# Optimization experiments

Hardware: AMD Instinct MI355X
Metric: run time of the kernel (lower is better)

## Reference

```python
import math
import jax, jax.numpy as jnp
import numpy as np

D_MODEL = 1024
NUM_HEADS = 16
HEAD_DIM = D_MODEL // NUM_HEADS
CAUSAL = True


def setup_inputs() -> dict:
    key = jax.random.key(0)
    ks = jax.random.split(key, 9)
    B, S = 2, 2048
    s = 1.0 / math.sqrt(D_MODEL)
    x = jax.random.normal(ks[0], (B, S, D_MODEL), dtype=jnp.float32)
    Wq = jax.random.normal(ks[1], (D_MODEL, D_MODEL), dtype=jnp.float32) * s
    bq = jax.random.normal(ks[2], (D_MODEL,), dtype=jnp.float32) * 0.01
    Wk = jax.random.normal(ks[3], (D_MODEL, D_MODEL), dtype=jnp.float32) * s
    bk = jax.random.normal(ks[4], (D_MODEL,), dtype=jnp.float32) * 0.01
    Wv = jax.random.normal(ks[5], (D_MODEL, D_MODEL), dtype=jnp.float32) * s
    bv = jax.random.normal(ks[6], (D_MODEL,), dtype=jnp.float32) * 0.01
    Wo = jax.random.normal(ks[7], (D_MODEL, D_MODEL), dtype=jnp.float32) * s
    bo = jax.random.normal(ks[8], (D_MODEL,), dtype=jnp.float32) * 0.01
    return {"x": x, "Wq": Wq, "bq": bq, "Wk": Wk, "bk": bk,
            "Wv": Wv, "bv": bv, "Wo": Wo, "bo": bo}


def reference(x, Wq, bq, Wk, bk, Wv, bv, Wo, bo):
    B, S, _ = x.shape
    # projections (torch Linear: x @ W.T + b; here W already stored as [in,out])
    q = x @ Wq + bq
    k = x @ Wk + bk
    v = x @ Wv + bv
    # split heads -> [B, H, S, hd]
    def split(t):
        return t.reshape(B, S, NUM_HEADS, HEAD_DIM).transpose(0, 2, 1, 3)
    q, k, v = split(q), split(k), split(v)
    scores = jnp.einsum('bhqd,bhkd->bhqk', q, k) / math.sqrt(HEAD_DIM)
    if CAUSAL:
        causal = jnp.tril(jnp.ones((S, S), dtype=bool))  # True = keep
        scores = jnp.where(causal, scores, -jnp.inf)
    attn = jax.nn.softmax(scores, axis=-1)
    out = jnp.einsum('bhqk,bhkd->bhqd', attn, v)
    out = out.transpose(0, 2, 1, 3).reshape(B, S, D_MODEL)
    return out @ Wo + bo
```

## Files before the change

### kernel.cpp

```cpp
#include <hip/hip_runtime.h>
#include <hip/hip_bf16.h>

typedef __bf16 bf16_t;
typedef __bf16 v8bf __attribute__((ext_vector_type(8)));
typedef float  v4f  __attribute__((ext_vector_type(4)));

#define MFMA16(a, b, c) __builtin_amdgcn_mfma_f32_16x16x32_bf16((a), (b), (c), 0, 0, 0)

#define GLDS16(g, l) __builtin_amdgcn_global_load_lds(                         \
    (const __attribute__((address_space(1))) void*)(g),                        \
    (__attribute__((address_space(3))) void*)(l), 16, 0, 0)

#define B_SZ   2
#define SEQ    2048
#define DM     1024
#define NH     16
#define HD     64
#define M_TOT  4096

#define QSCALE 0.18033688011112043f

__global__ __launch_bounds__(256)
void conv_x_kernel(const float* __restrict__ src, bf16_t* __restrict__ dst)
{
    int i = (blockIdx.x * 256 + threadIdx.x) * 8;
    float4 a = *reinterpret_cast<const float4*>(src + i);
    float4 b = *reinterpret_cast<const float4*>(src + i + 4);
    union { bf16_t h[8]; int4 v; } u;
    u.h[0] = (bf16_t)a.x; u.h[1] = (bf16_t)a.y; u.h[2] = (bf16_t)a.z; u.h[3] = (bf16_t)a.w;
    u.h[4] = (bf16_t)b.x; u.h[5] = (bf16_t)b.y; u.h[6] = (bf16_t)b.z; u.h[7] = (bf16_t)b.w;
    *reinterpret_cast<int4*>(dst + i) = u.v;
}

__global__ __launch_bounds__(256)
void conv_wt_kernel(const float* __restrict__ Wq, const float* __restrict__ Wk,
                    const float* __restrict__ Wv, const float* __restrict__ Wo,
                    bf16_t* __restrict__ WqkvT, bf16_t* __restrict__ WoT)
{
    __shared__ float t[32][33];
    const int z = blockIdx.z;
    const float* src = (z == 0) ? Wq : (z == 1) ? Wk : (z == 2) ? Wv : Wo;
    bf16_t* dst = (z < 3) ? (WqkvT + (size_t)z * 1048576) : WoT;
    const int tx = threadIdx.x & 31, ty = threadIdx.x >> 5;
    const int c0 = blockIdx.x * 32, r0 = blockIdx.y * 32;
#pragma unroll
    for (int i = 0; i < 4; ++i)
        t[ty + i * 8][tx] = src[(size_t)(r0 + ty + i * 8) * DM + c0 + tx];
    __syncthreads();
#pragma unroll
    for (int i = 0; i < 4; ++i)
        dst[(size_t)(c0 + ty + i * 8) * DM + r0 + tx] = (bf16_t)t[tx][ty + i * 8];
}

__global__ __launch_bounds__(256)
void gemm_qkv_kernel(const bf16_t* __restrict__ A, const bf16_t* __restrict__ BT,
                     const float* __restrict__ b0, const float* __restrict__ b1,
                     const float* __restrict__ b2,
                     bf16_t* __restrict__ oQ, bf16_t* __restrict__ oK,
                     bf16_t* __restrict__ oV)
{
    __shared__ __align__(16) bf16_t As[2 * 128 * 64];
    __shared__ __align__(16) bf16_t Bs[2 * 128 * 64];

    const int tid  = threadIdx.x;
    const int lane = tid & 63;
    const int wave = tid >> 6;
    const int wm   = (wave >> 1) * 64;
    const int wn   = (wave & 1) * 64;
    const int quad = lane >> 4;
    const int l15  = lane & 15;
    const int l7   = l15 & 7;

    const int mat = blockIdx.x >> 3;
    const int n0  = (blockIdx.x & 7) * 128;
    const int m0  = blockIdx.y * 128;
    const bf16_t* Bmat = BT + (size_t)mat * 1048576;

    const bf16_t *ap[4], *bp[4];
#pragma unroll
    for (int i = 0; i < 4; ++i) {
        int cidx = (wave * 4 + i) * 64 + lane;
        int r = cidx >> 3;
        int c = (cidx & 7) ^ (r & 7);
        ap[i] = A    + (size_t)(m0 + r) * DM + c * 8;
        bp[i] = Bmat + (size_t)(n0 + r) * DM + c * 8;
    }

    const v4f vzero = {0.f, 0.f, 0.f, 0.f};
    v4f acc[4][4];
#pragma unroll
    for (int mt = 0; mt < 4; ++mt)
#pragma unroll
        for (int nt = 0; nt < 4; ++nt) acc[mt][nt] = vzero;

#pragma unroll
    for (int i = 0; i < 4; ++i) {
        GLDS16(ap[i], As + (wave * 4 + i) * 512);
        GLDS16(bp[i], Bs + (wave * 4 + i) * 512);
        ap[i] += 64; bp[i] += 64;
    }

    for (int it = 0; it < 16; ++it) {
        const int cur = it & 1, nxt = cur ^ 1;
        __syncthreads();
        if (it < 15) {
#pragma unroll
            for (int i = 0; i < 4; ++i) {
                GLDS16(ap[i], As + nxt * 8192 + (wave * 4 + i) * 512);
                GLDS16(bp[i], Bs + nxt * 8192 + (wave * 4 + i) * 512);
                ap[i] += 64; bp[i] += 64;
            }
        }
#pragma unroll
        for (int ks = 0; ks < 2; ++ks) {
            v8bf af[4], bfq[4];
#pragma unroll
            for (int mt = 0; mt < 4; ++mt)
                af[mt] = *reinterpret_cast<const v8bf*>(
                    &As[cur * 8192 + (wm + mt * 16 + l15) * 64 + ((ks * 4 + quad) ^ l7) * 8]);
#pragma unroll
            for (int nt = 0; nt < 4; ++nt)
                bfq[nt] = *reinterpret_cast<const v8bf*>(
                    &Bs[cur * 8192 + (wn + nt * 16 + l15) * 64 + ((ks * 4 + quad) ^ l7) * 8]);
#pragma unroll
            for (int mt = 0; mt < 4; ++mt)
#pragma unroll
                for (int nt = 0; nt < 4; ++nt)
                    acc[mt][nt] = MFMA16(bfq[nt], af[mt], acc[mt][nt]);
        }
    }

    const float* bias = (mat == 0) ? b0 : (mat == 1) ? b1 : b2;
    if (mat != 2) {
        bf16_t* dst = (mat == 0) ? oQ : oK;
        const float scale = (mat == 0) ? QSCALE : 1.0f;
        const int h = (n0 + wn) >> 6;
#pragma unroll
        for (int nt = 0; nt < 4; ++nt) {
            const int dbase = nt * 16 + quad * 4;
            float4 bv = *reinterpret_cast<const float4*>(bias + n0 + wn + dbase);
#pragma unroll
            for (int mt = 0; mt < 4; ++mt) {
                int srow = m0 + wm + mt * 16 + l15;
                int b = srow >> 11, s = srow & 2047;
                union { bf16_t hh[4]; int2 v; } u;
                u.hh[0] = (bf16_t)((acc[mt][nt][0] + bv.x) * scale);
                u.hh[1] = (bf16_t)((acc[mt][nt][1] + bv.y) * scale);
                u.hh[2] = (bf16_t)((acc[mt][nt][2] + bv.z) * scale);
                u.hh[3] = (bf16_t)((acc[mt][nt][3] + bv.w) * scale);
                *reinterpret_cast<int2*>(
                    dst + ((size_t)(b * NH + h) * SEQ + s) * HD + dbase) = u.v;
            }
        }
    } else {
#pragma unroll
        for (int nt = 0; nt < 4; ++nt) {
#pragma unroll
            for (int r = 0; r < 4; ++r) {
                int coln = n0 + wn + nt * 16 + quad * 4 + r;
                float bv = bias[coln];
                int h = coln >> 6, d = coln & 63;
#pragma unroll
                for (int mt = 0; mt < 4; ++mt) {
                    int srow = m0 + wm + mt * 16 + l15;
                    int b = srow >> 11, s = srow & 2047;
                    oV[((size_t)(b * NH + h) * HD + d) * SEQ + s] =
                        (bf16_t)(acc[mt][nt][r] + bv);
                }
            }
        }
    }
}

__global__ __launch_bounds__(256)
void gemm_o_kernel(const bf16_t* __restrict__ A, const bf16_t* __restrict__ BT,
                   const float* __restrict__ bias, float* __restrict__ out)
{
    __shared__ __align__(16) bf16_t As[2 * 128 * 64];
    __shared__ __align__(16) bf16_t Bs[2 * 64 * 64];

    const int tid  = threadIdx.x;
    const int lane = tid & 63;
    const int wave = tid >> 6;
    const int wm   = (wave >> 1) * 64;
    const int wn   = (wave & 1) * 32;
    const int quad = lane >> 4;
    const int l15  = lane & 15;
    const int l7   = l15 & 7;

    const int n0 = blockIdx.x * 64;
    const int m0 = blockIdx.y * 128;

    const bf16_t *ap[4], *bp[2];
#pragma unroll
    for (int i = 0; i < 4; ++i) {
        int cidx = (wave * 4 + i) * 64 + lane;
        int r = cidx >> 3;
        int c = (cidx & 7) ^ (r & 7);
        ap[i] = A + (size_t)(m0 + r) * DM + c * 8;
    }
#pragma unroll
    for (int i = 0; i < 2; ++i) {
        int cidx = (wave * 2 + i) * 64 + lane;
        int r = cidx >> 3;
        int c = (cidx & 7) ^ (r & 7);
        bp[i] = BT + (size_t)(n0 + r) * DM + c * 8;
    }

    const v4f vzero = {0.f, 0.f, 0.f, 0.f};
    v4f acc[4][2];
#pragma unroll
    for (int mt = 0; mt < 4; ++mt)
#pragma unroll
        for (int nt = 0; nt < 2; ++nt) acc[mt][nt] = vzero;

#pragma unroll
    for (int i = 0; i < 4; ++i) { GLDS16(ap[i], As + (wave * 4 + i) * 512); ap[i] += 64; }
#pragma unroll
    for (int i = 0; i < 2; ++i) { GLDS16(bp[i], Bs + (wave * 2 + i) * 512); bp[i] += 64; }

    for (int it = 0; it < 16; ++it) {
        const int cur = it & 1, nxt = cur ^ 1;
        __syncthreads();
        if (it < 15) {
#pragma unroll
            for (int i = 0; i < 4; ++i) {
                GLDS16(ap[i], As + nxt * 8192 + (wave * 4 + i) * 512);
                ap[i] += 64;
            }
#pragma unroll
            for (int i = 0; i < 2; ++i) {
                GLDS16(bp[i], Bs + nxt * 4096 + (wave * 2 + i) * 512);
                bp[i] += 64;
            }
        }
#pragma unroll
        for (int ks = 0; ks < 2; ++ks) {
            v8bf af[4], bfq[2];
#pragma unroll
            for (int mt = 0; mt < 4; ++mt)
                af[mt] = *reinterpret_cast<const v8bf*>(
                    &As[cur * 8192 + (wm + mt * 16 + l15) * 64 + ((ks * 4 + quad) ^ l7) * 8]);
#pragma unroll
            for (int nt = 0; nt < 2; ++nt)
                bfq[nt] = *reinterpret_cast<const v8bf*>(
                    &Bs[cur * 4096 + (wn + nt * 16 + l15) * 64 + ((ks * 4 + quad) ^ l7) * 8]);
#pragma unroll
            for (int mt = 0; mt < 4; ++mt)
#pragma unroll
                for (int nt = 0; nt < 2; ++nt)
                    acc[mt][nt] = MFMA16(af[mt], bfq[nt], acc[mt][nt]);
        }
    }

#pragma unroll
    for (int mt = 0; mt < 4; ++mt) {
#pragma unroll
        for (int nt = 0; nt < 2; ++nt) {
            int col = n0 + wn + nt * 16 + l15;
            float bv = bias[col];
#pragma unroll
            for (int r = 0; r < 4; ++r) {
                int row = m0 + wm + mt * 16 + quad * 4 + r;
                out[(size_t)row * DM + col] = acc[mt][nt][r] + bv;
            }
        }
    }
}

__global__ __launch_bounds__(256)
void attn_kernel(const bf16_t* __restrict__ Q, const bf16_t* __restrict__ K,
                 const bf16_t* __restrict__ Vt, bf16_t* __restrict__ O)
{
    __shared__ __align__(16) bf16_t Ks[2][64 * 64];
    __shared__ __align__(16) bf16_t Vs[2][64 * 64];
    __shared__ __align__(16) bf16_t Ps[64 * 72];

    const int tid  = threadIdx.x;
    const int lane = tid & 63;
    const int w    = tid >> 6;
    const int quad = lane >> 4;
    const int l15  = lane & 15;
    const int l7   = lane & 7;

    const int p  = blockIdx.x;
    const int bh = blockIdx.y;
    const size_t base = (size_t)bh * SEQ * HD;
    const bf16_t* Qg = Q  + base;
    const bf16_t* Kg = K  + base;
    const bf16_t* Vg = Vt + base;

    const int rr0 = tid >> 3;
    const int cc0 = (tid & 7) ^ (rr0 & 7);
    const int bO = bh >> 4, hO = bh & 15;
    const v4f vzero = {0.f, 0.f, 0.f, 0.f};

    for (int phase = 0; phase < 2; ++phase) {
        const int t  = phase ? (31 - p) : p;
        const int q0 = t * 64;
        const int qg = q0 + w * 16 + l15;

        v8bf qf[2];
        {
            const bf16_t* qrow = Qg + (size_t)qg * HD;
            qf[0] = *reinterpret_cast<const v8bf*>(qrow + quad * 8);
            qf[1] = *reinterpret_cast<const v8bf*>(qrow + 32 + quad * 8);
        }

        const bf16_t* kp0 = Kg + (size_t)rr0 * HD + cc0 * 8;
        const bf16_t* kp1 = kp0 + 32 * HD;
        const bf16_t* vp0 = Vg + (size_t)rr0 * SEQ + cc0 * 8;
        const bf16_t* vp1 = vp0 + (size_t)32 * SEQ;

        v4f acc_o[4];
#pragma unroll
        for (int dt = 0; dt < 4; ++dt) acc_o[dt] = vzero;
        float lrow = 0.f;

        __syncthreads();
        GLDS16(kp0, &Ks[0][w * 512]);
        GLDS16(kp1, &Ks[0][2048 + w * 512]);
        GLDS16(vp0, &Vs[0][w * 512]);
        GLDS16(vp1, &Vs[0][2048 + w * 512]);
        kp0 += 64 * HD;  kp1 += 64 * HD;  vp0 += 64;  vp1 += 64;

        for (int kt = 0; kt <= t; ++kt) {
            const int cur = kt & 1, nxt = cur ^ 1;
            __syncthreads();
            if (kt < t) {
                GLDS16(kp0, &Ks[nxt][w * 512]);
                GLDS16(kp1, &Ks[nxt][2048 + w * 512]);
                GLDS16(vp0, &Vs[nxt][w * 512]);
                GLDS16(vp1, &Vs[nxt][2048 + w * 512]);
                kp0 += 64 * HD;  kp1 += 64 * HD;  vp0 += 64;  vp1 += 64;
            }

            v4f st[4];
#pragma unroll
            for (int ktile = 0; ktile < 4; ++ktile) st[ktile] = vzero;
#pragma unroll
            for (int ks = 0; ks < 2; ++ks) {
                v8bf kb[4];
#pragma unroll
                for (int ktile = 0; ktile < 4; ++ktile)
                    kb[ktile] = *reinterpret_cast<const v8bf*>(
                        &Ks[cur][(ktile * 16 + l15) * 64 + ((ks * 4 + quad) ^ l7) * 8]);
#pragma unroll
                for (int ktile = 0; ktile < 4; ++ktile)
                    st[ktile] = MFMA16(kb[ktile], qf[ks], st[ktile]);
            }

            const bool diagI = (kt == t);
            float rs = 0.f;
            const int prow = (w * 16 + l15) * 72;
#pragma unroll
            for (int ktile = 0; ktile < 4; ++ktile) {
                union { bf16_t h[4]; int2 v; } u;
                if (diagI && ktile > w) {
                    u.v.x = 0; u.v.y = 0;
                } else if (diagI && ktile == w) {
#pragma unroll
                    for (int r = 0; r < 4; ++r) {
                        int kg = kt * 64 + ktile * 16 + quad * 4 + r;
                        float pv = (kg > qg) ? 0.f : __builtin_amdgcn_exp2f(st[ktile][r]);
                        rs += pv;
                        u.h[r] = (bf16_t)pv;
                    }
                } else {
#pragma unroll
                    for (int r = 0; r < 4; ++r) {
                        float pv = __builtin_amdgcn_exp2f(st[ktile][r]);
                        rs += pv;
                        u.h[r] = (bf16_t)pv;
                    }
                }
                *reinterpret_cast<int2*>(&Ps[prow + ktile * 16 + quad * 4]) = u.v;
            }
            rs += __shfl_xor(rs, 16);
            rs += __shfl_xor(rs, 32);
            lrow += rs;

#pragma unroll
            for (int ks = 0; ks < 2; ++ks) {
                v8bf vb[4];
#pragma unroll
                for (int dt = 0; dt < 4; ++dt)
                    vb[dt] = *reinterpret_cast<const v8bf*>(
                        &Vs[cur][(dt * 16 + l15) * 64 + ((ks * 4 + quad) ^ l7) * 8]);
                v8bf pf = *reinterpret_cast<const v8bf*>(
                    &Ps[(w * 16 + l15) * 72 + ks * 32 + quad * 8]);
#pragma unroll
                for (int dt = 0; dt < 4; ++dt)
                    acc_o[dt] = MFMA16(vb[dt], pf, acc_o[dt]);
            }
        }

        float rinv = 1.f / lrow;
        int s = q0 + w * 16 + l15;
#pragma unroll
        for (int dt = 0; dt < 4; ++dt) {
            union { bf16_t h[4]; int2 v; } u;
#pragma unroll
            for (int r = 0; r < 4; ++r)
                u.h[r] = (bf16_t)(acc_o[dt][r] * rinv);
            *reinterpret_cast<int2*>(
                &O[((size_t)bO * SEQ + s) * DM + hO * 64 + dt * 16 + quad * 4]) = u.v;
        }
    }
}

extern "C" void kernel_launch(void* const* d_in, const int* in_sizes, int n_in,
                              void* d_out, int out_size, void* d_ws, size_t ws_size,
                              hipStream_t stream) {
    const float* x  = (const float*)d_in[0];
    const float* Wq = (const float*)d_in[1];
    const float* bq = (const float*)d_in[2];
    const float* Wk = (const float*)d_in[3];
    const float* bk = (const float*)d_in[4];
    const float* Wv = (const float*)d_in[5];
    const float* bv = (const float*)d_in[6];
    const float* Wo = (const float*)d_in[7];
    const float* bo = (const float*)d_in[8];

    bf16_t* ws = (bf16_t*)d_ws;
    bf16_t* xb     = ws;
    bf16_t* WqkvT  = ws + 4194304;
    bf16_t* WoT    = ws + 7340032;
    bf16_t* Qb     = ws + 8388608;
    bf16_t* Kb     = ws + 12582912;
    bf16_t* Vb     = ws + 16777216;
    bf16_t* Ob     = ws;

    conv_x_kernel<<<2048, 256, 0, stream>>>(x, xb);
    conv_wt_kernel<<<dim3(32, 32, 4), 256, 0, stream>>>(Wq, Wk, Wv, Wo, WqkvT, WoT);
    gemm_qkv_kernel<<<dim3(24, 32), 256, 0, stream>>>(xb, WqkvT, bq, bk, bv, Qb, Kb, Vb);
    attn_kernel<<<dim3(16, 32), 256, 0, stream>>>(Qb, Kb, Vb, Ob);
    gemm_o_kernel<<<dim3(16, 32), 256, 0, stream>>>(Ob, WoT, bo, (float*)d_out);
}
```

Measured before the change: 195.0 us.

## Deepen global-to-LDS prefetch with explicit vmcnt waits and split barriers

Restructures the double-buffered K-loops in the QKV GEMM, output GEMM and attention kernels. Both buffers are prefetched before the loop, and each iteration waits with a partial s_waitcnt vmcnt so only the current tile must have landed. The refill of the consumed buffer is issued after a second barrier at the end of the iteration. The aim is to let global loads run across a full compute iteration instead of stalling at __syncthreads, which drains all outstanding loads. The cost is two barriers per iteration, and correctness depends on the hand-written vmcnt counts matching the number of loads issued.

```diff
diff --git a/kernel.cpp b/kernel.cpp
--- a/kernel.cpp
+++ b/kernel.cpp
@@ -10,6 +10,10 @@
 #define GLDS16(g, l) __builtin_amdgcn_global_load_lds(                         \
     (const __attribute__((address_space(1))) void*)(g),                        \
     (__attribute__((address_space(3))) void*)(l), 16, 0, 0)
+
+#define VMEMCNT(n) asm volatile("s_waitcnt vmcnt(" #n ")" ::: "memory")
+#define SBAR()     __builtin_amdgcn_s_barrier()
+#define SFENCE()   __builtin_amdgcn_sched_barrier(0)
 
 #define B_SZ   2
 #define SEQ    2048
@@ -99,18 +103,17 @@
         GLDS16(bp[i], Bs + (wave * 4 + i) * 512);
         ap[i] += 64; bp[i] += 64;
     }
+#pragma unroll
+    for (int i = 0; i < 4; ++i) {
+        GLDS16(ap[i], As + 8192 + (wave * 4 + i) * 512);
+        GLDS16(bp[i], Bs + 8192 + (wave * 4 + i) * 512);
+        ap[i] += 64; bp[i] += 64;
+    }
 
     for (int it = 0; it < 16; ++it) {
-        const int cur = it & 1, nxt = cur ^ 1;
-        __syncthreads();
-        if (it < 15) {
-#pragma unroll
-            for (int i = 0; i < 4; ++i) {
-                GLDS16(ap[i], As + nxt * 8192 + (wave * 4 + i) * 512);
-                GLDS16(bp[i], Bs + nxt * 8192 + (wave * 4 + i) * 512);
-                ap[i] += 64; bp[i] += 64;
-            }
-        }
+        const int cur = it & 1;
+        if (it < 15) { VMEMCNT(8); } else { VMEMCNT(0); }
+        SBAR(); SFENCE();
 #pragma unroll
         for (int ks = 0; ks < 2; ++ks) {
             v8bf af[4], bfq[4];
@@ -127,6 +130,15 @@
 #pragma unroll
                 for (int nt = 0; nt < 4; ++nt)
                     acc[mt][nt] = MFMA16(bfq[nt], af[mt], acc[mt][nt]);
+        }
+        SFENCE(); SBAR();
+        if (it < 14) {
+#pragma unroll
+            for (int i = 0; i < 4; ++i) {
+                GLDS16(ap[i], As + cur * 8192 + (wave * 4 + i) * 512);
+                GLDS16(bp[i], Bs + cur * 8192 + (wave * 4 + i) * 512);
+                ap[i] += 64; bp[i] += 64;
+            }
         }
     }
 
@@ -218,22 +230,15 @@
     for (int i = 0; i < 4; ++i) { GLDS16(ap[i], As + (wave * 4 + i) * 512); ap[i] += 64; }
 #pragma unroll
     for (int i = 0; i < 2; ++i) { GLDS16(bp[i], Bs + (wave * 2 + i) * 512); bp[i] += 64; }
+#pragma unroll
+    for (int i = 0; i < 4; ++i) { GLDS16(ap[i], As + 8192 + (wave * 4 + i) * 512); ap[i] += 64; }
+#pragma unroll
+    for (int i = 0; i < 2; ++i) { GLDS16(bp[i], Bs + 4096 + (wave * 2 + i) * 512); bp[i] += 64; }
 
     for (int it = 0; it < 16; ++it) {
-        const int cur = it & 1, nxt = cur ^ 1;
-        __syncthreads();
-        if (it < 15) {
-#pragma unroll
-            for (int i = 0; i < 4; ++i) {
-                GLDS16(ap[i], As + nxt * 8192 + (wave * 4 + i) * 512);
-                ap[i] += 64;
-            }
-#pragma unroll
-            for (int i = 0; i < 2; ++i) {
-                GLDS16(bp[i], Bs + nxt * 4096 + (wave * 2 + i) * 512);
-                bp[i] += 64;
-            }
-        }
+        const int cur = it & 1;
+        if (it < 15) { VMEMCNT(6); } else { VMEMCNT(0); }
+        SBAR(); SFENCE();
 #pragma unroll
         for (int ks = 0; ks < 2; ++ks) {
             v8bf af[4], bfq[2];
@@ -250,6 +255,19 @@
 #pragma unroll
                 for (int nt = 0; nt < 2; ++nt)
                     acc[mt][nt] = MFMA16(af[mt], bfq[nt], acc[mt][nt]);
+        }
+        SFENCE(); SBAR();
+        if (it < 14) {
+#pragma unroll
+            for (int i = 0; i < 4; ++i) {
+                GLDS16(ap[i], As + cur * 8192 + (wave * 4 + i) * 512);
+                ap[i] += 64;
+            }
+#pragma unroll
+            for (int i = 0; i < 2; ++i) {
+                GLDS16(bp[i], Bs + cur * 4096 + (wave * 2 + i) * 512);
+                bp[i] += 64;
+            }
         }
     }
 
@@ -317,23 +335,25 @@
         for (int dt = 0; dt < 4; ++dt) acc_o[dt] = vzero;
         float lrow = 0.f;
 
-        __syncthreads();
+        VMEMCNT(0);
+        SBAR();
         GLDS16(kp0, &Ks[0][w * 512]);
         GLDS16(kp1, &Ks[0][2048 + w * 512]);
         GLDS16(vp0, &Vs[0][w * 512]);
         GLDS16(vp1, &Vs[0][2048 + w * 512]);
         kp0 += 64 * HD;  kp1 += 64 * HD;  vp0 += 64;  vp1 += 64;
+        if (t >= 1) {
+            GLDS16(kp0, &Ks[1][w * 512]);
+            GLDS16(kp1, &Ks[1][2048 + w * 512]);
+            GLDS16(vp0, &Vs[1][w * 512]);
+            GLDS16(vp1, &Vs[1][2048 + w * 512]);
+            kp0 += 64 * HD;  kp1 += 64 * HD;  vp0 += 64;  vp1 += 64;
+        }
 
         for (int kt = 0; kt <= t; ++kt) {
-            const int cur = kt & 1, nxt = cur ^ 1;
-            __syncthreads();
-            if (kt < t) {
-                GLDS16(kp0, &Ks[nxt][w * 512]);
-                GLDS16(kp1, &Ks[nxt][2048 + w * 512]);
-                GLDS16(vp0, &Vs[nxt][w * 512]);
-                GLDS16(vp1, &Vs[nxt][2048 + w * 512]);
-                kp0 += 64 * HD;  kp1 += 64 * HD;  vp0 += 64;  vp1 += 64;
-            }
+            const int cur = kt & 1;
+            if (kt < t) { VMEMCNT(4); } else { VMEMCNT(0); }
+            SBAR(); SFENCE();
 
             v4f st[4];
 #pragma unroll
@@ -392,6 +412,15 @@
 #pragma unroll
                 for (int dt = 0; dt < 4; ++dt)
                     acc_o[dt] = MFMA16(vb[dt], pf, acc_o[dt]);
+            }
+
+            SFENCE(); SBAR();
+            if (kt + 2 <= t) {
+                GLDS16(kp0, &Ks[cur][w * 512]);
+                GLDS16(kp1, &Ks[cur][2048 + w * 512]);
+                GLDS16(vp0, &Vs[cur][w * 512]);
+                GLDS16(vp1, &Vs[cur][2048 + w * 512]);
+                kp0 += 64 * HD;  kp1 += 64 * HD;  vp0 += 64;  vp1 += 64;
             }
         }
 
```

Result: no change. 192.5 us (-1.3%).
